# Performance work log

Hardware: AMD Instinct MI355X
Metric: run time of the kernel (lower is better)

## Reference

```python
import jax, jax.numpy as jnp
import numpy as np

B, CIN, NH, W, L, K = 16, 64, 64, 32, 4, 5
EPS = 1e-5
FORGET_BIAS = 1.0


def conv(x, w, b=None):
    # x: [B,C,H,W], w: [O,I,k,k] -> SAME padding, stride 1 (NCHW)
    y = jax.lax.conv_general_dilated(x, w, (1, 1), 'SAME',
                                     dimension_numbers=('NCHW', 'OIHW', 'NCHW'))
    if b is not None:
        y = y + b[None, :, None, None]
    return y


def ln(x, g, b):
    # torch LayerNorm([C,W,W]): normalize each sample over (C,H,W)
    m = jnp.mean(x, axis=(1, 2, 3), keepdims=True)
    v = jnp.mean((x - m) ** 2, axis=(1, 2, 3), keepdims=True)
    return (x - m) * jax.lax.rsqrt(v + EPS) * g[None] + b[None]


def attn_channel(q, kv):
    # q: [B,C,W,H], kv: [B,L,C,W,H]
    b, c, w, h = q.shape
    qf = q.reshape(b, c, w * h)                 # [B,C,HW]
    kf = kv.reshape(b, -1, w * h)               # [B,L*C,HW]
    a = jax.nn.softmax(jnp.einsum('bcp,blp->bcl', qf, kf), axis=2)  # [B,C,L*C]
    out = jnp.einsum('bcl,blp->bcp', a, kf)     # [B,C,HW]
    return out.reshape(b, c, w, h)


def attn_spatial(q, kv):
    # q: [B,C,W,H], kv: [B,L,C,W,H]
    b, c, w, h = q.shape
    qf = q.reshape(b, c, w * h).transpose(0, 2, 1)          # [B,HW,C]
    kf = kv.transpose(0, 1, 3, 4, 2).reshape(b, -1, c)      # [B,L*HW,C]
    a = jax.nn.softmax(jnp.einsum('bpc,bqc->bpq', qf, kf), axis=2)  # [B,HW,L*HW]
    out = jnp.einsum('bpq,bqc->bpc', a, kf)                 # [B,HW,C]
    return out.reshape(b, w, h, c).transpose(0, 3, 1, 2)


def setup_inputs() -> dict:
    key = jax.random.key(0)
    ks = iter(jax.random.split(key, 64))
    rn = lambda shape, s=1.0: jax.random.normal(next(ks), shape, jnp.float32) * s
    ones = lambda shape: jnp.ones(shape, jnp.float32)
    zeros = lambda shape: jnp.zeros(shape, jnp.float32)
    s = 0.02
    d = {}
    d['x_t'] = rn((B, CIN, W, W))
    d['h_t'] = rn((B, NH, W, W))
    d['c_t'] = rn((B, NH, W, W))
    d['c_historys'] = rn((B, L, NH, W, W))
    d['m_t'] = rn((B, NH, W, W))
    d['w_x'] = rn((7 * NH, CIN, K, K), s); d['ln_x_g'] = ones((7 * NH, W, W)); d['ln_x_b'] = zeros((7 * NH, W, W))
    d['w_h'] = rn((4 * NH, NH, K, K), s);  d['ln_h_g'] = ones((4 * NH, W, W)); d['ln_h_b'] = zeros((4 * NH, W, W))
    d['w_m'] = rn((3 * NH, NH, K, K), s);  d['ln_m_g'] = ones((3 * NH, W, W)); d['ln_m_b'] = zeros((3 * NH, W, W))
    d['w_o'] = rn((NH, 2 * NH, K, K), s);  d['ln_o_g'] = ones((NH, W, W));     d['ln_o_b'] = zeros((NH, W, W))
    d['w_last'] = rn((NH, 2 * NH, 1, 1), s)
    d['s_norm_g'] = ones((NH, W, W)); d['s_norm_b'] = zeros((NH, W, W))
    d['c_norm_g'] = ones((NH, W, W)); d['c_norm_b'] = zeros((NH, W, W))
    d['ca_w1'] = rn((NH, NH, K, K), s); d['ca_b1'] = zeros((NH,))
    d['ca_ln_g'] = ones((NH, W, W));    d['ca_ln_b'] = zeros((NH, W, W))
    d['ca_w2'] = rn((NH, NH, 1, 1), s); d['ca_b2'] = zeros((NH,))
    d['sa_w1'] = rn((NH, NH, K, K), s)
    d['sa_ln_g'] = ones((NH, W, W));    d['sa_ln_b'] = zeros((NH, W, W))
    d['sa_w2'] = rn((NH, NH, 1, 1), s)
    d['attn_w'] = rn((NH, NH, 1, 1), s)
    return d


def reference(x_t, h_t, c_t, c_historys, m_t,
              w_x, ln_x_g, ln_x_b, w_h, ln_h_g, ln_h_b, w_m, ln_m_g, ln_m_b,
              w_o, ln_o_g, ln_o_b, w_last,
              s_norm_g, s_norm_b, c_norm_g, c_norm_b,
              ca_w1, ca_b1, ca_ln_g, ca_ln_b, ca_w2, ca_b2,
              sa_w1, sa_ln_g, sa_ln_b, sa_w2, attn_w):
    x_concat = ln(conv(x_t, w_x), ln_x_g, ln_x_b)
    h_concat = ln(conv(h_t, w_h), ln_h_g, ln_h_b)
    m_concat = ln(conv(m_t, w_m), ln_m_g, ln_m_b)
    (i_x, f_x, g_x, i_xp, f_xp, g_xp, o_x) = jnp.split(x_concat, 7, axis=1)
    (i_h, f_h, g_h, o_h) = jnp.split(h_concat, 4, axis=1)
    (i_m, f_m, g_m) = jnp.split(m_concat, 3, axis=1)

    i_t = jax.nn.sigmoid(i_x + i_h)
    f_t = jax.nn.sigmoid(f_x + f_h + FORGET_BIAS)
    g_t = jnp.tanh(g_x + g_h)

    # attn_sum_fussion(c_t, query=f_t, keys=c_historys, values=c_historys)
    sp = ln(c_t + attn_spatial(f_t, c_historys), s_norm_g, s_norm_b)
    ch = ln(c_t + attn_channel(f_t, c_historys), c_norm_g, c_norm_b)
    s_a = conv(jax.nn.relu(ln(conv(sp, sa_w1), sa_ln_g, sa_ln_b)), sa_w2)
    c_a = conv(jax.nn.relu(ln(conv(ch, ca_w1, ca_b1), ca_ln_g, ca_ln_b)), ca_w2, ca_b2)
    attn = conv(s_a + c_a, attn_w)
    c_new = attn + i_t * g_t

    i_tp = jax.nn.sigmoid(i_xp + i_m)
    f_tp = jax.nn.sigmoid(f_xp + f_m + FORGET_BIAS)
    g_tp = jnp.tanh(g_xp + g_m)
    m_new = f_tp * m_t + i_tp * g_tp

    mem = jnp.concatenate((c_new, m_new), axis=1)
    o_t = jax.nn.sigmoid(o_x + o_h + ln(conv(mem, w_o), ln_o_g, ln_o_b))
    h_new = o_t * jnp.tanh(conv(mem, w_last))
    return h_new, c_new, m_new
```

## Files before the change

### kernel.cpp

```cpp
#include <hip/hip_runtime.h>
#include <hip/hip_bf16.h>

#define N1 (1u << 20)

typedef __attribute__((ext_vector_type(8))) short s8v;
typedef __attribute__((ext_vector_type(4))) float f4v;

static __device__ __forceinline__ float sigm(float x){ return 1.f/(1.f + __expf(-x)); }
static __device__ __forceinline__ float tanh_(float x){ return 1.f - 2.f/(__expf(2.f*x) + 1.f); }

static __device__ __forceinline__ ushort f2b(float f){
  union { float f; uint u; } x; x.f = f;
  uint r = x.u + 0x7FFFu + ((x.u >> 16) & 1u);
  return (ushort)(r >> 16);
}

static __device__ __forceinline__ void red_atomic2(float s, float q, float* d, int b, int t){
  #pragma unroll
  for (int m = 32; m; m >>= 1){ s += __shfl_xor(s, m); q += __shfl_xor(q, m); }
  if ((t & 63) == 0){ atomicAdd(&d[b*2], s); atomicAdd(&d[b*2+1], q); }
}

__global__ void k_zero(float* __restrict__ p){ p[threadIdx.x] = 0.f; }

__global__ __launch_bounds__(256) void k_wprep3(
    const float* __restrict__ sA, ushort* __restrict__ dA, int CoA, int CiA, int nA,
    const float* __restrict__ sB, ushort* __restrict__ dB, int CoB, int CiB, int nB,
    const float* __restrict__ sC, ushort* __restrict__ dC, int CoC, int CiC, int nC)
{
  int idx = blockIdx.x*256 + threadIdx.x;
  const float* s; ushort* d; int Co, Ci;
  if (idx < nA){ s=sA; d=dA; Co=CoA; Ci=CiA; }
  else if ((idx -= nA) < nB){ s=sB; d=dB; Co=CoB; Ci=CiB; }
  else if ((idx -= nB) < nC){ s=sC; d=dC; Co=CoC; Ci=CiC; }
  else return;
  int ci = idx % Ci; int r = idx / Ci; int co = r % Co; int tap = r / Co;
  d[idx] = f2b(s[((size_t)(co*Ci + ci))*25 + tap]);
}

struct PT { const float* s; ushort* d; const float* st; const float* g; const float* bb; };

__global__ __launch_bounds__(256) void k_prepT3(PT ja, PT jb, PT jc, int n0, int n1, float invN)
{
  const int lp = blockIdx.y;
  PT j; int pl;
  if (lp < n0){ j = ja; pl = lp; }
  else if (lp < n0 + n1){ j = jb; pl = lp - n0; }
  else { j = jc; pl = lp - n0 - n1; }
  const float* sp = j.s + ((size_t)pl << 16);
  float mean = 0.f, rstd = 0.f;
  if (j.st){
    float s0 = j.st[pl*2], s1 = j.st[pl*2+1];
    mean = s0*invN; rstd = rsqrtf(s1*invN - mean*mean + 1e-5f);
  }
  const int p0 = blockIdx.x << 6;
  __shared__ __align__(16) float T[64][68];
  const int t = threadIdx.x, c = t >> 2, g4 = t & 3;
  #pragma unroll
  for (int i = 0; i < 4; ++i){
    const int px = (g4 << 4) + (i << 2);
    float4 f = *(const float4*)(sp + ((size_t)c << 10) + p0 + px);
    if (j.st){
      const size_t li = ((size_t)c << 10) + p0 + px;
      float4 gv = *(const float4*)(j.g + li);
      float4 bv = *(const float4*)(j.bb + li);
      f.x = (f.x - mean)*rstd*gv.x + bv.x;
      f.y = (f.y - mean)*rstd*gv.y + bv.y;
      f.z = (f.z - mean)*rstd*gv.z + bv.z;
      f.w = (f.w - mean)*rstd*gv.w + bv.w;
    }
    *(float4*)&T[c][px] = f;
  }
  __syncthreads();
  const int p = t >> 2, c0 = (t & 3) << 4;
  uint w4[8];
  #pragma unroll
  for (int k = 0; k < 8; ++k){
    ushort lo = f2b(T[c0 + 2*k][p]);
    ushort hi = f2b(T[c0 + 2*k + 1][p]);
    w4[k] = (uint)lo | ((uint)hi << 16);
  }
  ushort* dst = j.d + ((((size_t)pl << 10) + p0 + p) << 6) + c0;
  *(uint4*)(dst)     = *(uint4*)&w4[0];
  *(uint4*)(dst + 8) = *(uint4*)&w4[4];
}

__global__ __launch_bounds__(256) void k_prepTm(const float* __restrict__ src, ushort* __restrict__ dT)
{
  const int lp = blockIdx.y;
  const int p0 = blockIdx.x << 6;
  const float* sp = src + ((size_t)lp << 16);
  __shared__ __align__(16) float T[64][68];
  const int t = threadIdx.x, c = t >> 2, g4 = t & 3;
  #pragma unroll
  for (int i = 0; i < 4; ++i){
    const int px = (g4 << 4) + (i << 2);
    *(float4*)&T[c][px] = *(const float4*)(sp + ((size_t)c << 10) + p0 + px);
  }
  __syncthreads();
  const int p = t >> 2, c0 = (t & 3) << 4;
  uint w4[8];
  #pragma unroll
  for (int k = 0; k < 8; ++k)
    w4[k] = (uint)f2b(T[c0 + 2*k][p]) | ((uint)f2b(T[c0 + 2*k + 1][p]) << 16);
  ushort* dst = dT + ((((size_t)(lp >> 1) << 10) + p0 + p) << 7) + ((lp & 1) << 6) + c0;
  *(uint4*)(dst)     = *(uint4*)&w4[0];
  *(uint4*)(dst + 8) = *(uint4*)&w4[4];
}

struct Seg {
  const ushort* inT; const ushort* w; const float* bias;
  float* out; float* ostat;
  int Cin, Cout;
};
struct Segs3 { Seg s[3]; int b1, b2; };

template<int MT>
__global__ __launch_bounds__(256, MT==4 ? 2 : 3) void k_convX(Segs3 Sg)
{
  constexpr int CO   = MT*16;
  constexpr int NW   = 5*CO*4;
  constexpr int ITW  = (NW + 255) / 256;
  constexpr int DXSH = (MT == 4 ? 8 : 7);

  const int b = blockIdx.y;
  const int cog = blockIdx.x >> 2, pxblk = blockIdx.x & 3;
  const int si = (cog >= Sg.b1) + (cog >= Sg.b2);
  const Seg sg = Sg.s[si];
  const int base = si == 0 ? 0 : (si == 1 ? Sg.b1 : Sg.b2);
  const int co0 = (cog - base) * CO;
  const int r0 = pxblk << 3;
  const int t = threadIdx.x, w = t >> 6, l = t & 63;
  const int lane16 = l & 15, quad = l >> 4;

  __shared__ __align__(16) ushort S_[4][12][36][8];
  __shared__ __align__(16) ushort W_[2][5*CO*32];

  f4v acc[MT][4];
  #pragma unroll
  for (int mi = 0; mi < MT; ++mi)
    #pragma unroll
    for (int n = 0; n < 4; ++n) acc[mi][n] = (f4v){0.f,0.f,0.f,0.f};

  size_t woff0[ITW];
  #pragma unroll
  for (int it = 0; it < ITW; ++it){
    const int u = t + it*256;
    const int l16u = u & 15, qu = (u >> 4) & 3;
    const int miu = (u >> 6) & (MT - 1), dxu = u >> DXSH;
    woff0[it] = ((size_t)(dxu*sg.Cout + co0 + miu*16 + l16u))*sg.Cin + (qu << 3);
  }
  const size_t wdy = (size_t)5 * sg.Cout * sg.Cin;

  const int ncc = sg.Cin >> 5;
  for (int cc = 0; cc < ncc; ++cc){
    __syncthreads();
    for (int idx = t; idx < 432; idx += 256){
      const int row = idx / 36, col = idx - row*36;
      const int ir = r0 - 2 + row, ic = col - 2;
      uint4 pk[4] = {make_uint4(0,0,0,0),make_uint4(0,0,0,0),make_uint4(0,0,0,0),make_uint4(0,0,0,0)};
      if ((unsigned)ir < 32u && (unsigned)ic < 32u){
        const ushort* bp = sg.inT + ((size_t)((b << 10) + (ir << 5) + ic)) * sg.Cin + (cc << 5);
        #pragma unroll
        for (int q = 0; q < 4; ++q) pk[q] = *(const uint4*)(bp + (q << 3));
      }
      #pragma unroll
      for (int q = 0; q < 4; ++q) *(uint4*)&S_[q][row][col][0] = pk[q];
    }
    {
      uint4 wreg[ITW];
      #pragma unroll
      for (int it = 0; it < ITW; ++it)
        if (ITW*256 == NW || t + it*256 < NW)
          wreg[it] = *(const uint4*)(sg.w + woff0[it] + (cc << 5));
      #pragma unroll
      for (int it = 0; it < ITW; ++it)
        if (ITW*256 == NW || t + it*256 < NW)
          *(uint4*)&W_[0][(size_t)(t + it*256) * 8] = wreg[it];
    }
    __syncthreads();
    #pragma unroll
    for (int dy = 0; dy < 5; ++dy){
      uint4 nreg[ITW];
      if (dy < 4){
        #pragma unroll
        for (int it = 0; it < ITW; ++it)
          if (ITW*256 == NW || t + it*256 < NW)
            nreg[it] = *(const uint4*)(sg.w + woff0[it] + (size_t)(dy+1)*wdy + (cc << 5));
      }
      #pragma unroll
      for (int dx = 0; dx < 5; ++dx){
        s8v a[MT];
        #pragma unroll
        for (int mi = 0; mi < MT; ++mi){
          const int au = ((((dx*MT + mi) << 2) + quad) << 4) + lane16;
          a[mi] = *(const s8v*)&W_[dy & 1][au << 3];
        }
        #pragma unroll
        for (int n = 0; n < 4; ++n){
          const int srow = (w << 1) + (n >> 1) + dy;
          const int col = ((n & 1) << 4) + lane16 + dx;
          s8v bb = *(const s8v*)&S_[quad][srow][col][0];
          #pragma unroll
          for (int mi = 0; mi < MT; ++mi)
            acc[mi][n] = __builtin_amdgcn_mfma_f32_16x16x32_bf16(a[mi], bb, acc[mi][n], 0, 0, 0);
        }
      }
      if (dy < 4){
        #pragma unroll
        for (int it = 0; it < ITW; ++it)
          if (ITW*256 == NW || t + it*256 < NW)
            *(uint4*)&W_[(dy+1) & 1][(size_t)(t + it*256) * 8] = nreg[it];
      }
      __syncthreads();
    }
  }
  float lsum = 0.f, lsq = 0.f;
  #pragma unroll
  for (int mi = 0; mi < MT; ++mi){
    const int co = co0 + mi*16 + (quad << 2);
    #pragma unroll
    for (int n = 0; n < 4; ++n){
      const int row = r0 + (w << 1) + (n >> 1);
      const int col = ((n & 1) << 4) + lane16;
      #pragma unroll
      for (int i = 0; i < 4; ++i){
        float v = acc[mi][n][i] + (sg.bias ? sg.bias[co+i] : 0.f);
        sg.out[(((size_t)(b*sg.Cout + co + i)) << 10) + (row << 5) + col] = v;
        lsum += v; lsq += v*v;
      }
    }
  }
  if (sg.ostat) red_atomic2(lsum, lsq, sg.ostat, b, t);
}

__global__ __launch_bounds__(256) void k_prep(const float* __restrict__ src,
                                              ushort* __restrict__ outC,
                                              ushort* __restrict__ outT)
{
  const int plane = blockIdx.y;
  const int p0 = blockIdx.x << 6;
  const float* sp = src + ((size_t)plane << 16);
  __shared__ __align__(16) float T[64][68];
  const int t = threadIdx.x, c = t >> 2, g = t & 3;
  #pragma unroll
  for (int i = 0; i < 4; ++i){
    float4 f = *(const float4*)(sp + ((size_t)c << 10) + p0 + (g << 4) + (i << 2));
    *(float4*)&T[c][(g << 4) + (i << 2)] = f;
    if (outC){
      uint2 pk2;
      pk2.x = (uint)f2b(f.x) | ((uint)f2b(f.y) << 16);
      pk2.y = (uint)f2b(f.z) | ((uint)f2b(f.w) << 16);
      *(uint2*)(outC + ((((size_t)plane << 6) + c) << 10) + p0 + (g << 4) + (i << 2)) = pk2;
    }
  }
  __syncthreads();
  const int p = t >> 2, c0 = (t & 3) << 4;
  uint w4[8];
  #pragma unroll
  for (int k = 0; k < 8; ++k){
    ushort lo = f2b(T[c0 + 2*k][p]);
    ushort hi = f2b(T[c0 + 2*k + 1][p]);
    w4[k] = (uint)lo | ((uint)hi << 16);
  }
  ushort* dst = outT + ((((size_t)plane << 10) + p0 + p) << 6) + c0;
  *(uint4*)(dst)     = *(uint4*)&w4[0];
  *(uint4*)(dst + 8) = *(uint4*)&w4[4];
}

__global__ __launch_bounds__(256) void k_gates(
    const float* __restrict__ bufx, const float* __restrict__ bufh, const float* __restrict__ bufm,
    const float* __restrict__ lnxg, const float* __restrict__ lnxb,
    const float* __restrict__ lnhg, const float* __restrict__ lnhb,
    const float* __restrict__ lnmg, const float* __restrict__ lnmb,
    const float* __restrict__ m_t, const float* __restrict__ stats,
    float* __restrict__ ft, float* __restrict__ ig, float* __restrict__ osum,
    float* __restrict__ memo, float* __restrict__ out_m)
{
  const int idx = blockIdx.x*256 + threadIdx.x;
  const int b = idx >> 16, rem = idx & 65535;
  const int c = rem >> 10, p = rem & 1023;

  float mx = stats[b*2]      * (1.f/458752.f);
  float vx = stats[b*2+1]    * (1.f/458752.f) - mx*mx;  float rx = rsqrtf(vx + 1e-5f);
  float mh = stats[32+b*2]   * (1.f/262144.f);
  float vh = stats[32+b*2+1] * (1.f/262144.f) - mh*mh;  float rh = rsqrtf(vh + 1e-5f);
  float mm = stats[64+b*2]   * (1.f/196608.f);
  float vm = stats[64+b*2+1] * (1.f/196608.f) - mm*mm;  float rm = rsqrtf(vm + 1e-5f);

  auto LX = [&](int k){
    size_t ch = (size_t)k*64 + c; size_t gi = ((size_t)b*448 + ch)*1024 + p; size_t li = ch*1024 + p;
    return (bufx[gi] - mx)*rx*lnxg[li] + lnxb[li]; };
  auto LH = [&](int k){
    size_t ch = (size_t)k*64 + c; size_t gi = ((size_t)b*256 + ch)*1024 + p; size_t li = ch*1024 + p;
    return (bufh[gi] - mh)*rh*lnhg[li] + lnhb[li]; };
  auto LM = [&](int k){
    size_t ch = (size_t)k*64 + c; size_t gi = ((size_t)b*192 + ch)*1024 + p; size_t li = ch*1024 + p;
    return (bufm[gi] - mm)*rm*lnmg[li] + lnmb[li]; };

  float i_t = sigm(LX(0) + LH(0));
  float f_t = sigm(LX(1) + LH(1) + 1.f);
  float g_t = tanh_(LX(2) + LH(2));
  float i_p = sigm(LX(3) + LM(0));
  float f_p = sigm(LX(4) + LM(1) + 1.f);
  float g_p = tanh_(LX(5) + LM(2));
  float ox = LX(6), oh = LH(3);

  ft[idx]   = f_t;
  ig[idx]   = i_t * g_t;
  osum[idx] = ox + oh;
  float mn = f_p * m_t[idx] + i_p * g_p;
  out_m[idx] = mn;
  memo[((size_t)(b*128 + 64 + c) << 10) + p] = mn;
}

__global__ __launch_bounds__(256) void k_spat_mfma(
    const ushort* __restrict__ qT, const ushort* __restrict__ kvC, const ushort* __restrict__ kvT,
    float* __restrict__ num0, float* __restrict__ num1, float* __restrict__ den)
{
  const int p0 = blockIdx.x << 6, b = blockIdx.y, half = blockIdx.z;
  const int t = threadIdx.x, w = t >> 6, l = t & 63;
  const int lane16 = l & 15, quad = l >> 4;
  __shared__ __align__(16) ushort Kt[64][72];
  __shared__ __align__(16) ushort Kc[64][72];
  __shared__ __align__(16) ushort Eb[64][72];
  __shared__ __align__(16) float  XO[64][65];

  s8v qa0, qa1;
  {
    const ushort* qr = qT + ((((size_t)b << 10) + p0 + (w << 4) + lane16) << 6) + (quad << 3);
    qa0 = *(const s8v*)(qr);
    qa1 = *(const s8v*)(qr + 32);
  }
  f4v o0 = {0.f,0.f,0.f,0.f}, o1 = o0, o2 = o0, o3 = o0, dacc = o0;
  const short oneb = (short)0x3F80;
  const s8v ones = { oneb, oneb, oneb, oneb, oneb, oneb, oneb, oneb };

  const int r = t >> 2, g4 = (t & 3) << 4;
  for (int ck = 0; ck < 32; ++ck){
    const int chunk = (half << 5) + ck;
    const int lidx = chunk >> 4, pk = (chunk & 15) << 6;
    __syncthreads();
    {
      const ushort* sc = kvC + ((((size_t)(b*4 + lidx) << 6) + r) << 10) + pk + g4;
      *(uint4*)&Kc[r][g4]     = *(const uint4*)(sc);
      *(uint4*)&Kc[r][g4 + 8] = *(const uint4*)(sc + 8);
      const ushort* st = kvT + ((((size_t)(b*4 + lidx) << 10) + pk + r) << 6) + g4;
      *(uint4*)&Kt[r][g4]     = *(const uint4*)(st);
      *(uint4*)&Kt[r][g4 + 8] = *(const uint4*)(st + 8);
    }
    __syncthreads();
    #pragma unroll
    for (int nt = 0; nt < 4; ++nt){
      const ushort* bt = &Kt[(nt << 4) + lane16][quad << 3];
      s8v b0 = *(const s8v*)(bt);
      s8v b1 = *(const s8v*)(bt + 32);
      f4v s = {0.f,0.f,0.f,0.f};
      s = __builtin_amdgcn_mfma_f32_16x16x32_bf16(qa0, b0, s, 0, 0, 0);
      s = __builtin_amdgcn_mfma_f32_16x16x32_bf16(qa1, b1, s, 0, 0, 0);
      #pragma unroll
      for (int i = 0; i < 4; ++i){
        float e = __expf(s[i] - 12.f);
        Eb[(w << 4) + (quad << 2) + i][(nt << 4) + lane16] = f2b(e);
      }
    }
    __syncthreads();
    #pragma unroll
    for (int ks = 0; ks < 2; ++ks){
      s8v ea = *(const s8v*)&Eb[(w << 4) + lane16][(ks << 5) + (quad << 3)];
      dacc = __builtin_amdgcn_mfma_f32_16x16x32_bf16(ea, ones, dacc, 0, 0, 0);
      s8v bc0 = *(const s8v*)&Kc[ 0 + lane16][(ks << 5) + (quad << 3)];
      s8v bc1 = *(const s8v*)&Kc[16 + lane16][(ks << 5) + (quad << 3)];
      s8v bc2 = *(const s8v*)&Kc[32 + lane16][(ks << 5) + (quad << 3)];
      s8v bc3 = *(const s8v*)&Kc[48 + lane16][(ks << 5) + (quad << 3)];
      o0 = __builtin_amdgcn_mfma_f32_16x16x32_bf16(ea, bc0, o0, 0, 0, 0);
      o1 = __builtin_amdgcn_mfma_f32_16x16x32_bf16(ea, bc1, o1, 0, 0, 0);
      o2 = __builtin_amdgcn_mfma_f32_16x16x32_bf16(ea, bc2, o2, 0, 0, 0);
      o3 = __builtin_amdgcn_mfma_f32_16x16x32_bf16(ea, bc3, o3, 0, 0, 0);
    }
  }
  {
    const int pxl = (w << 4) + (quad << 2);
    if (lane16 == 0){
      float* dp = den + (((size_t)(half*16 + b)) << 10) + p0 + pxl;
      dp[0] = dacc[0]; dp[1] = dacc[1]; dp[2] = dacc[2]; dp[3] = dacc[3];
    }
    XO[ 0 + lane16][pxl+0] = o0[0]; XO[ 0 + lane16][pxl+1] = o0[1];
    XO[ 0 + lane16][pxl+2] = o0[2]; XO[ 0 + lane16][pxl+3] = o0[3];
    XO[16 + lane16][pxl+0] = o1[0]; XO[16 + lane16][pxl+1] = o1[1];
    XO[16 + lane16][pxl+2] = o1[2]; XO[16 + lane16][pxl+3] = o1[3];
    XO[32 + lane16][pxl+0] = o2[0]; XO[32 + lane16][pxl+1] = o2[1];
    XO[32 + lane16][pxl+2] = o2[2]; XO[32 + lane16][pxl+3] = o2[3];
    XO[48 + lane16][pxl+0] = o3[0]; XO[48 + lane16][pxl+1] = o3[1];
    XO[48 + lane16][pxl+2] = o3[2]; XO[48 + lane16][pxl+3] = o3[3];
  }
  __syncthreads();
  {
    const int ch = t >> 2;
    float* nout = half ? num1 : num0;
    #pragma unroll
    for (int i = 0; i < 4; ++i){
      size_t gi = ((size_t)b << 16) + ((size_t)ch << 10) + p0 + g4 + (i << 2);
      float4 ov;
      ov.x = XO[ch][g4 + (i << 2) + 0];
      ov.y = XO[ch][g4 + (i << 2) + 1];
      ov.z = XO[ch][g4 + (i << 2) + 2];
      ov.w = XO[ch][g4 + (i << 2) + 3];
      *(float4*)(nout + gi) = ov;
    }
  }
}

__global__ __launch_bounds__(256) void k_spcomb(
    const float* num0, const float* num1, const float* __restrict__ den,
    const float* __restrict__ c_t, float* sp_raw, float* __restrict__ stats)
{
  const int p0 = blockIdx.x << 6, b = blockIdx.y, t = threadIdx.x;
  const int ch = t >> 2, g4 = (t & 3) << 4;
  float lsum = 0.f, lsq = 0.f;
  #pragma unroll
  for (int i = 0; i < 4; ++i){
    const int px = p0 + g4 + (i << 2);
    size_t gi = ((size_t)b << 16) + ((size_t)ch << 10) + px;
    float4 n0 = *(const float4*)(num0 + gi);
    float4 n1 = *(const float4*)(num1 + gi);
    float4 cv = *(const float4*)(c_t + gi);
    const float* d0 = den + (((size_t)b) << 10) + px;
    const float* d1 = den + (((size_t)(16 + b)) << 10) + px;
    float4 ov;
    ov.x = cv.x + (n0.x + n1.x) / (d0[0] + d1[0]);
    ov.y = cv.y + (n0.y + n1.y) / (d0[1] + d1[1]);
    ov.z = cv.z + (n0.z + n1.z) / (d0[2] + d1[2]);
    ov.w = cv.w + (n0.w + n1.w) / (d0[3] + d1[3]);
    *(float4*)(sp_raw + gi) = ov;
    lsum += ov.x + ov.y + ov.z + ov.w;
    lsq  += ov.x*ov.x + ov.y*ov.y + ov.z*ov.z + ov.w*ov.w;
  }
  red_atomic2(lsum, lsq, stats, b, t);
}

__global__ __launch_bounds__(256) void k_chlog_m(
    const ushort* __restrict__ ftC, const ushort* __restrict__ kvC, float* __restrict__ lg)
{
  const int bx = blockIdx.x, b = blockIdx.y;
  const int np = bx >> 1, mp = bx & 1;
  const int t = threadIdx.x, w = t >> 6, l = t & 63;
  const int lane16 = l & 15, quad = l >> 4;
  __shared__ __align__(16) ushort As[8][32][8];
  __shared__ __align__(16) ushort Bs[8][64][8];
  f4v acc[2];
  acc[0] = (f4v){0.f,0.f,0.f,0.f}; acc[1] = (f4v){0.f,0.f,0.f,0.f};

  for (int kc = 0; kc < 16; ++kc){
    __syncthreads();
    {
      const int c = t >> 3, q = t & 7;
      *(uint4*)&As[q][c][0] = *(const uint4*)(ftC + (((size_t)(b*64 + mp*32 + c)) << 10) + (kc<<6) + (q<<3));
    }
    #pragma unroll
    for (int it = 0; it < 2; ++it){
      const int idx = t + it*256;
      const int r2 = idx >> 3, q = idx & 7;
      *(uint4*)&Bs[q][r2][0] = *(const uint4*)(kvC + ((((size_t)(b*4 + np) << 6) + r2) << 10) + (kc<<6) + (q<<3));
    }
    __syncthreads();
    #pragma unroll
    for (int ks = 0; ks < 2; ++ks){
      s8v a0 = *(const s8v*)&As[(ks<<2)+quad][lane16][0];
      s8v a1 = *(const s8v*)&As[(ks<<2)+quad][16 + lane16][0];
      s8v bb = *(const s8v*)&Bs[(ks<<2)+quad][(w<<4) + lane16][0];
      acc[0] = __builtin_amdgcn_mfma_f32_16x16x32_bf16(a0, bb, acc[0], 0, 0, 0);
      acc[1] = __builtin_amdgcn_mfma_f32_16x16x32_bf16(a1, bb, acc[1], 0, 0, 0);
    }
  }
  #pragma unroll
  for (int mi = 0; mi < 2; ++mi)
    #pragma unroll
    for (int i = 0; i < 4; ++i){
      const int c = mp*32 + mi*16 + (quad<<2) + i;
      const int n = (np<<6) + (w<<4) + lane16;
      lg[(((size_t)(b*64 + c)) << 8) + n] = acc[mi][i];
    }
}

__global__ __launch_bounds__(256) void k_chsm(const float* __restrict__ a, ushort* __restrict__ ab)
{
  const int row  = blockIdx.x*4 + (threadIdx.x >> 6);
  const int lane = threadIdx.x & 63;
  const float* rp = a + ((size_t)row << 8);
  float v0 = rp[lane], v1 = rp[lane+64], v2 = rp[lane+128], v3 = rp[lane+192];
  float mx = fmaxf(fmaxf(v0, v1), fmaxf(v2, v3));
  #pragma unroll
  for (int m = 32; m; m >>= 1) mx = fmaxf(mx, __shfl_xor(mx, m));
  v0 = __expf(v0 - mx); v1 = __expf(v1 - mx); v2 = __expf(v2 - mx); v3 = __expf(v3 - mx);
  float s = v0 + v1 + v2 + v3;
  #pragma unroll
  for (int m = 32; m; m >>= 1) s += __shfl_xor(s, m);
  float inv = 1.f / s;
  ushort* op = ab + ((size_t)row << 8);
  op[lane] = f2b(v0*inv); op[lane+64] = f2b(v1*inv);
  op[lane+128] = f2b(v2*inv); op[lane+192] = f2b(v3*inv);
}

__global__ __launch_bounds__(256) void k_chout_m(
    const ushort* __restrict__ chlb, const ushort* __restrict__ kvT,
    const float* __restrict__ c_t, float* __restrict__ ch_raw, float* __restrict__ stats)
{
  const int p0 = blockIdx.x << 6, b = blockIdx.y;
  const int t = threadIdx.x, w = t >> 6, l = t & 63;
  const int lane16 = l & 15, quad = l >> 4;
  __shared__ __align__(16) ushort As[32][64][8];
  __shared__ __align__(16) ushort Bs[32][32][8];
  #pragma unroll
  for (int it = 0; it < 8; ++it){
    const int idx = t + it*256;
    const int c = idx >> 5, q = idx & 31;
    *(uint4*)&As[q][c][0] = *(const uint4*)(chlb + (((size_t)(b*64 + c)) << 8) + (q<<3));
  }
  __syncthreads();
  s8v a[8];
  #pragma unroll
  for (int ks = 0; ks < 8; ++ks)
    a[ks] = *(const s8v*)&As[(ks<<2)+quad][(w<<4) + lane16][0];
  float lsum = 0.f, lsq = 0.f;
  for (int pc = 0; pc < 2; ++pc){
    __syncthreads();
    #pragma unroll
    for (int it = 0; it < 4; ++it){
      const int idx = t + it*256;
      const int px = idx >> 5, q = idx & 31;
      const int plane = (b<<2) + (q>>3);
      *(uint4*)&Bs[q][px][0] = *(const uint4*)(kvT + ((((size_t)plane << 10) + p0 + (pc<<5) + px) << 6) + ((q&7)<<3));
    }
    __syncthreads();
    #pragma unroll
    for (int nt = 0; nt < 2; ++nt){
      f4v o = {0.f,0.f,0.f,0.f};
      #pragma unroll
      for (int ks = 0; ks < 8; ++ks){
        s8v bb = *(const s8v*)&Bs[(ks<<2)+quad][(nt<<4) + lane16][0];
        o = __builtin_amdgcn_mfma_f32_16x16x32_bf16(a[ks], bb, o, 0, 0, 0);
      }
      #pragma unroll
      for (int i = 0; i < 4; ++i){
        const int c = (w<<4) + (quad<<2) + i;
        const int px = p0 + (pc<<5) + (nt<<4) + lane16;
        size_t gi = ((size_t)b << 16) + ((size_t)c << 10) + px;
        float v = c_t[gi] + o[i];
        ch_raw[gi] = v;
        lsum += v; lsq += v*v;
      }
    }
  }
  red_atomic2(lsum, lsq, stats, b, t);
}

__global__ __launch_bounds__(256) void k_attnfinal(
    const float* __restrict__ samid, const float* __restrict__ camid,
    const float* __restrict__ stats_sa, const float* __restrict__ stats_ca,
    const float* __restrict__ salng, const float* __restrict__ salnb,
    const float* __restrict__ calng, const float* __restrict__ calnb,
    const float* __restrict__ wsa2, const float* __restrict__ wca2,
    const float* __restrict__ cab2, const float* __restrict__ wat,
    const float* __restrict__ ig, float* __restrict__ out_c, float* __restrict__ memo)
{
  const int p0 = blockIdx.x << 6, b = blockIdx.y, t = threadIdx.x;
  const int tc = t & 15, tp = t >> 4;
  __shared__ __align__(16) float R[64][68];
  __shared__ __align__(16) float Wl[64][68];
  __shared__ __align__(16) float Ms[64][68];
  const float invN = 1.f/65536.f;
  float acc[4][4] = {};
  #pragma unroll
  for (int pass = 0; pass < 2; ++pass){
    const float* mid = pass ? camid : samid;
    const float* st  = pass ? stats_ca : stats_sa;
    const float* g   = pass ? calng : salng;
    const float* bb  = pass ? calnb : salnb;
    const float* w   = pass ? wca2  : wsa2;
    float mean = st[b*2]*invN;
    float var  = st[b*2+1]*invN - mean*mean;
    float rstd = rsqrtf(var + 1e-5f);
    __syncthreads();
    {
      const int j = t & 63, c0 = t >> 6;
      for (int ci = c0; ci < 64; ci += 4){
        size_t gi = ((size_t)b << 16) + ((size_t)ci << 10) + p0 + j;
        size_t li = ((size_t)ci << 10) + p0 + j;
        float v = (mid[gi] - mean)*rstd*g[li] + bb[li];
        R[ci][j] = fmaxf(v, 0.f);
      }
      const int ci2 = t & 63, c20 = t >> 6;
      for (int c2 = c20; c2 < 64; c2 += 4) Wl[ci2][c2] = w[((size_t)c2 << 6) + ci2];
    }
    __syncthreads();
    for (int ci = 0; ci < 64; ++ci){
      float wv[4], rv[4];
      *(float4*)wv = *(const float4*)&Wl[ci][4*tc];
      *(float4*)rv = *(const float4*)&R[ci][4*tp];
      #pragma unroll
      for (int i = 0; i < 4; ++i)
        #pragma unroll
        for (int j = 0; j < 4; ++j)
          acc[i][j] = fmaf(wv[i], rv[j], acc[i][j]);
    }
  }
  {
    float b2[4];
    #pragma unroll
    for (int i = 0; i < 4; ++i) b2[i] = cab2[4*tc + i];
    #pragma unroll
    for (int i = 0; i < 4; ++i)
      #pragma unroll
      for (int j = 0; j < 4; ++j)
        Ms[4*tc+i][4*tp+j] = acc[i][j] + b2[i];
  }
  __syncthreads();
  {
    const int ci2 = t & 63, c20 = t >> 6;
    for (int c2 = c20; c2 < 64; c2 += 4) Wl[ci2][c2] = wat[((size_t)c2 << 6) + ci2];
  }
  __syncthreads();
  float acc2[4][4] = {};
  for (int c2 = 0; c2 < 64; ++c2){
    float wv[4], mv[4];
    *(float4*)wv = *(const float4*)&Wl[c2][4*tc];
    *(float4*)mv = *(const float4*)&Ms[c2][4*tp];
    #pragma unroll
    for (int i = 0; i < 4; ++i)
      #pragma unroll
      for (int j = 0; j < 4; ++j)
        acc2[i][j] = fmaf(wv[i], mv[j], acc2[i][j]);
  }
  #pragma unroll
  for (int i = 0; i < 4; ++i)
    #pragma unroll
    for (int j = 0; j < 4; ++j){
      size_t gi = ((size_t)b << 16) + ((size_t)(4*tc + i) << 10) + p0 + 4*tp + j;
      float v = acc2[i][j] + ig[gi];
      out_c[gi] = v;
      memo[((size_t)(b*128 + 4*tc + i) << 10) + p0 + 4*tp + j] = v;
    }
}

__global__ __launch_bounds__(256) void k_final(
    const float* __restrict__ memo, const float* __restrict__ wlast,
    const float* __restrict__ bufo, const float* __restrict__ osum,
    const float* __restrict__ stats_o, const float* __restrict__ lnog, const float* __restrict__ lnob,
    float* __restrict__ out_h)
{
  const int p0 = blockIdx.x << 6, b = blockIdx.y, t = threadIdx.x;
  const int tc = t & 15, tp = t >> 4;
  __shared__ __align__(16) float Msh[64][68];
  __shared__ __align__(16) float Wt[64][68];
  float acc[4][4] = {};
  #pragma unroll
  for (int half = 0; half < 2; ++half){
    __syncthreads();
    {
      const int j = t & 63, c0 = t >> 6;
      for (int ci = c0; ci < 64; ci += 4)
        Msh[ci][j] = memo[((size_t)(b*128 + half*64 + ci) << 10) + p0 + j];
      const int ci2 = t & 63, co0 = t >> 6;
      for (int co = co0; co < 64; co += 4) Wt[ci2][co] = wlast[((size_t)co << 7) + half*64 + ci2];
    }
    __syncthreads();
    for (int ci = 0; ci < 64; ++ci){
      float wv[4], mv[4];
      *(float4*)wv = *(const float4*)&Wt[ci][4*tc];
      *(float4*)mv = *(const float4*)&Msh[ci][4*tp];
      #pragma unroll
      for (int i = 0; i < 4; ++i)
        #pragma unroll
        for (int j = 0; j < 4; ++j)
          acc[i][j] = fmaf(wv[i], mv[j], acc[i][j]);
    }
  }
  float mean = stats_o[b*2]*(1.f/65536.f);
  float var  = stats_o[b*2+1]*(1.f/65536.f) - mean*mean;
  float rstd = rsqrtf(var + 1e-5f);
  #pragma unroll
  for (int i = 0; i < 4; ++i)
    #pragma unroll
    for (int j = 0; j < 4; ++j){
      const int co = 4*tc + i, p = p0 + 4*tp + j;
      size_t gi = ((size_t)b << 16) + ((size_t)co << 10) + p;
      size_t li = ((size_t)co << 10) + p;
      float lno = (bufo[gi] - mean)*rstd*lnog[li] + lnob[li];
      float o = sigm(osum[gi] + lno);
      out_h[gi] = o * tanh_(acc[i][j]);
    }
}

extern "C" void kernel_launch(void* const* d_in, const int* in_sizes, int n_in,
                              void* d_out, int out_size, void* d_ws, size_t ws_size,
                              hipStream_t stream)
{
  const float* x_t   = (const float*)d_in[0];
  const float* h_t   = (const float*)d_in[1];
  const float* c_t   = (const float*)d_in[2];
  const float* chist = (const float*)d_in[3];
  const float* m_t   = (const float*)d_in[4];
  const float* w_x   = (const float*)d_in[5];
  const float* lnxg  = (const float*)d_in[6];
  const float* lnxb  = (const float*)d_in[7];
  const float* w_h   = (const float*)d_in[8];
  const float* lnhg  = (const float*)d_in[9];
  const float* lnhb  = (const float*)d_in[10];
  const float* w_m   = (const float*)d_in[11];
  const float* lnmg  = (const float*)d_in[12];
  const float* lnmb  = (const float*)d_in[13];
  const float* w_o   = (const float*)d_in[14];
  const float* lnog  = (const float*)d_in[15];
  const float* lnob  = (const float*)d_in[16];
  const float* w_last= (const float*)d_in[17];
  const float* sng   = (const float*)d_in[18];
  const float* snb   = (const float*)d_in[19];
  const float* cng   = (const float*)d_in[20];
  const float* cnb   = (const float*)d_in[21];
  const float* ca_w1 = (const float*)d_in[22];
  const float* ca_b1 = (const float*)d_in[23];
  const float* calng = (const float*)d_in[24];
  const float* calnb = (const float*)d_in[25];
  const float* ca_w2 = (const float*)d_in[26];
  const float* ca_b2 = (const float*)d_in[27];
  const float* sa_w1 = (const float*)d_in[28];
  const float* salng = (const float*)d_in[29];
  const float* salnb = (const float*)d_in[30];
  const float* sa_w2 = (const float*)d_in[31];
  const float* attn_w= (const float*)d_in[32];

  float* out = (float*)d_out;
  float* ws  = (float*)d_ws;

  float* stats = ws;
  float* bufx  = ws + 1024;
  float* bufh  = bufx + 7*(size_t)N1;
  float* bufm  = bufh + 4*(size_t)N1;
  float* ft    = bufm + 3*(size_t)N1;
  float* ig    = ft   + (size_t)N1;
  float* osum  = ig   + (size_t)N1;
  float* memo  = osum + (size_t)N1;
  float* sp    = bufx;
  float* ch    = bufx + (size_t)N1;
  float* samid = bufx + 2*(size_t)N1;
  float* camid = bufx + 3*(size_t)N1;
  float* bufo  = bufx + 4*(size_t)N1;
  float* chl   = bufx + 5*(size_t)N1;
  ushort* kvC  = (ushort*)bufh;
  ushort* kvT  = kvC + 4*(size_t)N1;
  ushort* qT   = (ushort*)bufm;
  ushort* ftC  = qT + (size_t)N1;

  ushort* xT   = (ushort*)memo;
  ushort* hT   = xT + (size_t)N1;
  ushort* mT   = hT + (size_t)N1;
  ushort* spT  = ftC + (size_t)N1;
  ushort* chT  = spT + (size_t)N1;
  float*  num1 = bufm + 2*(size_t)N1;
  float*  denP = chl;
  ushort* memoT = (ushort*)bufx;

  ushort* wbx = (ushort*)ft;
  ushort* wbh = wbx + 716800;
  ushort* wbm = wbh + 409600;
  ushort* wbo  = (ushort*)(chl + 262144);
  ushort* wbsa = wbo + 204800;
  ushort* wbca = wbsa + 102400;
  ushort* chlb = wbca + 102400;

  float* out_h = out;
  float* out_c = out + (size_t)N1;
  float* out_m = out + 2*(size_t)N1;

  k_zero<<<dim3(1), dim3(256), 0, stream>>>(stats);

  k_wprep3<<<dim3(5600), dim3(256), 0, stream>>>(
      w_x, wbx, 448, 64, 716800,
      w_h, wbh, 256, 64, 409600,
      w_m, wbm, 192, 64, 307200);

  {
    PT jx{ x_t, xT, nullptr, nullptr, nullptr };
    PT jh{ h_t, hT, nullptr, nullptr, nullptr };
    PT jm{ m_t, mT, nullptr, nullptr, nullptr };
    k_prepT3<<<dim3(16,48), dim3(256), 0, stream>>>(jx, jh, jm, 16, 16, 0.f);
  }

  {
    Segs3 XHM;
    XHM.s[0] = Seg{ xT, wbx, nullptr, bufx, stats+0,  64, 448 };
    XHM.s[1] = Seg{ hT, wbh, nullptr, bufh, stats+32, 64, 256 };
    XHM.s[2] = Seg{ mT, wbm, nullptr, bufm, stats+64, 64, 192 };
    XHM.b1 = 7; XHM.b2 = 11;
    k_convX<4><<<dim3(56,16), dim3(256), 0, stream>>>(XHM);
  }

  k_gates<<<dim3(4096), dim3(256), 0, stream>>>(bufx, bufh, bufm, lnxg, lnxb, lnhg, lnhb,
                                                lnmg, lnmb, m_t, stats,
                                                ft, ig, osum, memo, out_m);

  k_wprep3<<<dim3(1600), dim3(256), 0, stream>>>(
      w_o,   wbo,  64, 128, 204800,
      sa_w1, wbsa, 64,  64, 102400,
      ca_w1, wbca, 64,  64, 102400);

  k_prep<<<dim3(16,64), dim3(256), 0, stream>>>(chist, kvC, kvT);
  k_prep<<<dim3(16,16), dim3(256), 0, stream>>>(ft, ftC, qT);

  k_spat_mfma<<<dim3(16,16,2), dim3(256), 0, stream>>>(qT, kvC, kvT, sp, num1, denP);
  k_spcomb<<<dim3(16,16), dim3(256), 0, stream>>>(sp, num1, denP, c_t, sp, stats+96);

  k_chlog_m<<<dim3(8,16), dim3(256), 0, stream>>>(ftC, kvC, chl);
  k_chsm  <<<dim3(256),  dim3(256), 0, stream>>>(chl, chlb);
  k_chout_m<<<dim3(16,16), dim3(256), 0, stream>>>(chlb, kvT, c_t, ch, stats+128);

  {
    PT js{ sp, spT, stats+96,  sng, snb };
    PT jc{ ch, chT, stats+128, cng, cnb };
    k_prepT3<<<dim3(16,32), dim3(256), 0, stream>>>(js, jc, js, 16, 16, 1.f/65536.f);
  }

  {
    Segs3 SC;
    SC.s[0] = Seg{ spT, wbsa, nullptr, samid, stats+160, 64, 64 };
    SC.s[1] = Seg{ chT, wbca, ca_b1,   camid, stats+192, 64, 64 };
    SC.s[2] = SC.s[1];
    SC.b1 = 2; SC.b2 = 1000;
    k_convX<2><<<dim3(16,16), dim3(256), 0, stream>>>(SC);
  }

  k_attnfinal<<<dim3(16,16), dim3(256), 0, stream>>>(samid, camid, stats+160, stats+192,
                                                     salng, salnb, calng, calnb,
                                                     sa_w2, ca_w2, ca_b2, attn_w,
                                                     ig, out_c, memo);

  k_prepTm<<<dim3(16,32), dim3(256), 0, stream>>>(memo, memoT);

  {
    Segs3 O;
    O.s[0] = Seg{ memoT, wbo, nullptr, bufo, stats+224, 128, 64 };
    O.s[1] = O.s[0]; O.s[2] = O.s[0];
    O.b1 = 1000; O.b2 = 1000;
    k_convX<2><<<dim3(8,16), dim3(256), 0, stream>>>(O);
  }

  k_final<<<dim3(16,16), dim3(256), 0, stream>>>(memo, w_last, bufo, osum, stats+224,
                                                 lnog, lnob, out_h);
}
```

Measured before the change: 496.8 us.

## Increase grid parallelism for small convs and spatial attention, merge prep launches

Templates the conv kernel on rows-per-block so the two small 64-output convs run with half-height tiles and twice as many blocks. Splits the spatial attention key range four ways instead of two and sums the four partial numerators and denominators in the combine kernel. Folds the stats zeroing into the weight-prep kernel and merges the two transpose/prep launches into one. This targets under-filled GPUs and launch overhead, but costs more halo reloading per block and more partial-sum traffic and buffer space.

Result: no change. 501.7 us (+1.0%).

```diff
diff --git a/kernel.cpp b/kernel.cpp
--- a/kernel.cpp
+++ b/kernel.cpp
@@ -21,13 +21,13 @@
   if ((t & 63) == 0){ atomicAdd(&d[b*2], s); atomicAdd(&d[b*2+1], q); }
 }
 
-__global__ void k_zero(float* __restrict__ p){ p[threadIdx.x] = 0.f; }
-
 __global__ __launch_bounds__(256) void k_wprep3(
     const float* __restrict__ sA, ushort* __restrict__ dA, int CoA, int CiA, int nA,
     const float* __restrict__ sB, ushort* __restrict__ dB, int CoB, int CiB, int nB,
-    const float* __restrict__ sC, ushort* __restrict__ dC, int CoC, int CiC, int nC)
-{
+    const float* __restrict__ sC, ushort* __restrict__ dC, int CoC, int CiC, int nC,
+    float* __restrict__ zs)
+{
+  if (zs && blockIdx.x == 0) zs[threadIdx.x] = 0.f;
   int idx = blockIdx.x*256 + threadIdx.x;
   const float* s; ushort* d; int Co, Ci;
   if (idx < nA){ s=sA; d=dA; Co=CoA; Ci=CiA; }
@@ -115,32 +115,37 @@
 };
 struct Segs3 { Seg s[3]; int b1, b2; };
 
-template<int MT>
+template<int MT, int RPB>
 __global__ __launch_bounds__(256, MT==4 ? 2 : 3) void k_convX(Segs3 Sg)
 {
   constexpr int CO   = MT*16;
   constexpr int NW   = 5*CO*4;
   constexpr int ITW  = (NW + 255) / 256;
   constexpr int DXSH = (MT == 4 ? 8 : 7);
+  constexpr int PXB  = 32/RPB;
+  constexpr int ROWS = RPB + 4;
+  constexpr int RPW  = RPB/4;
+  constexpr int NTIL = RPB/2;
+  constexpr int SUN2 = ROWS*36;
 
   const int b = blockIdx.y;
-  const int cog = blockIdx.x >> 2, pxblk = blockIdx.x & 3;
+  const int cog = blockIdx.x / PXB, pxblk = blockIdx.x % PXB;
   const int si = (cog >= Sg.b1) + (cog >= Sg.b2);
   const Seg sg = Sg.s[si];
   const int base = si == 0 ? 0 : (si == 1 ? Sg.b1 : Sg.b2);
   const int co0 = (cog - base) * CO;
-  const int r0 = pxblk << 3;
+  const int r0 = pxblk * RPB;
   const int t = threadIdx.x, w = t >> 6, l = t & 63;
   const int lane16 = l & 15, quad = l >> 4;
 
-  __shared__ __align__(16) ushort S_[4][12][36][8];
+  __shared__ __align__(16) ushort S_[4][ROWS][36][8];
   __shared__ __align__(16) ushort W_[2][5*CO*32];
 
-  f4v acc[MT][4];
+  f4v acc[MT][NTIL];
   #pragma unroll
   for (int mi = 0; mi < MT; ++mi)
     #pragma unroll
-    for (int n = 0; n < 4; ++n) acc[mi][n] = (f4v){0.f,0.f,0.f,0.f};
+    for (int n = 0; n < NTIL; ++n) acc[mi][n] = (f4v){0.f,0.f,0.f,0.f};
 
   size_t woff0[ITW];
   #pragma unroll
@@ -155,7 +160,7 @@
   const int ncc = sg.Cin >> 5;
   for (int cc = 0; cc < ncc; ++cc){
     __syncthreads();
-    for (int idx = t; idx < 432; idx += 256){
+    for (int idx = t; idx < SUN2; idx += 256){
       const int row = idx / 36, col = idx - row*36;
       const int ir = r0 - 2 + row, ic = col - 2;
       uint4 pk[4] = {make_uint4(0,0,0,0),make_uint4(0,0,0,0),make_uint4(0,0,0,0),make_uint4(0,0,0,0)};
@@ -197,8 +202,8 @@
           a[mi] = *(const s8v*)&W_[dy & 1][au << 3];
         }
         #pragma unroll
-        for (int n = 0; n < 4; ++n){
-          const int srow = (w << 1) + (n >> 1) + dy;
+        for (int n = 0; n < NTIL; ++n){
+          const int srow = w*RPW + (n >> 1) + dy;
           const int col = ((n & 1) << 4) + lane16 + dx;
           s8v bb = *(const s8v*)&S_[quad][srow][col][0];
           #pragma unroll
@@ -220,8 +225,8 @@
   for (int mi = 0; mi < MT; ++mi){
     const int co = co0 + mi*16 + (quad << 2);
     #pragma unroll
-    for (int n = 0; n < 4; ++n){
-      const int row = r0 + (w << 1) + (n >> 1);
+    for (int n = 0; n < NTIL; ++n){
+      const int row = r0 + w*RPW + (n >> 1);
       const int col = ((n & 1) << 4) + lane16;
       #pragma unroll
       for (int i = 0; i < 4; ++i){
@@ -234,25 +239,26 @@
   if (sg.ostat) red_atomic2(lsum, lsq, sg.ostat, b, t);
 }
 
-__global__ __launch_bounds__(256) void k_prep(const float* __restrict__ src,
-                                              ushort* __restrict__ outC,
-                                              ushort* __restrict__ outT)
+__global__ __launch_bounds__(256) void k_prep2(
+    const float* __restrict__ sA, ushort* __restrict__ cA, ushort* __restrict__ tA, int nA,
+    const float* __restrict__ sB, ushort* __restrict__ cB, ushort* __restrict__ tB)
 {
   const int plane = blockIdx.y;
+  const float* src; ushort* outC; ushort* outT; int pl;
+  if (plane < nA){ src = sA; outC = cA; outT = tA; pl = plane; }
+  else { src = sB; outC = cB; outT = tB; pl = plane - nA; }
   const int p0 = blockIdx.x << 6;
-  const float* sp = src + ((size_t)plane << 16);
+  const float* sp = src + ((size_t)pl << 16);
   __shared__ __align__(16) float T[64][68];
   const int t = threadIdx.x, c = t >> 2, g = t & 3;
   #pragma unroll
   for (int i = 0; i < 4; ++i){
     float4 f = *(const float4*)(sp + ((size_t)c << 10) + p0 + (g << 4) + (i << 2));
     *(float4*)&T[c][(g << 4) + (i << 2)] = f;
-    if (outC){
-      uint2 pk2;
-      pk2.x = (uint)f2b(f.x) | ((uint)f2b(f.y) << 16);
-      pk2.y = (uint)f2b(f.z) | ((uint)f2b(f.w) << 16);
-      *(uint2*)(outC + ((((size_t)plane << 6) + c) << 10) + p0 + (g << 4) + (i << 2)) = pk2;
-    }
+    uint2 pk2;
+    pk2.x = (uint)f2b(f.x) | ((uint)f2b(f.y) << 16);
+    pk2.y = (uint)f2b(f.z) | ((uint)f2b(f.w) << 16);
+    *(uint2*)(outC + ((((size_t)pl << 6) + c) << 10) + p0 + (g << 4) + (i << 2)) = pk2;
   }
   __syncthreads();
   const int p = t >> 2, c0 = (t & 3) << 4;
@@ -263,7 +269,7 @@
     ushort hi = f2b(T[c0 + 2*k + 1][p]);
     w4[k] = (uint)lo | ((uint)hi << 16);
   }
-  ushort* dst = outT + ((((size_t)plane << 10) + p0 + p) << 6) + c0;
+  ushort* dst = outT + ((((size_t)pl << 10) + p0 + p) << 6) + c0;
   *(uint4*)(dst)     = *(uint4*)&w4[0];
   *(uint4*)(dst + 8) = *(uint4*)&w4[4];
 }
@@ -316,7 +322,7 @@
 
 __global__ __launch_bounds__(256) void k_spat_mfma(
     const ushort* __restrict__ qT, const ushort* __restrict__ kvC, const ushort* __restrict__ kvT,
-    float* __restrict__ num0, float* __restrict__ num1, float* __restrict__ den)
+    float* __restrict__ num, float* __restrict__ den)
 {
   const int p0 = blockIdx.x << 6, b = blockIdx.y, half = blockIdx.z;
   const int t = threadIdx.x, w = t >> 6, l = t & 63;
@@ -337,8 +343,8 @@
   const s8v ones = { oneb, oneb, oneb, oneb, oneb, oneb, oneb, oneb };
 
   const int r = t >> 2, g4 = (t & 3) << 4;
-  for (int ck = 0; ck < 32; ++ck){
-    const int chunk = (half << 5) + ck;
+  for (int ck = 0; ck < 16; ++ck){
+    const int chunk = (half << 4) + ck;
     const int lidx = chunk >> 4, pk = (chunk & 15) << 6;
     __syncthreads();
     {
@@ -397,7 +403,7 @@
   __syncthreads();
   {
     const int ch = t >> 2;
-    float* nout = half ? num1 : num0;
+    float* nout = num + (size_t)half * N1;
     #pragma unroll
     for (int i = 0; i < 4; ++i){
       size_t gi = ((size_t)b << 16) + ((size_t)ch << 10) + p0 + g4 + (i << 2);
@@ -412,7 +418,7 @@
 }
 
 __global__ __launch_bounds__(256) void k_spcomb(
-    const float* num0, const float* num1, const float* __restrict__ den,
+    const float* num, const float* __restrict__ den,
     const float* __restrict__ c_t, float* sp_raw, float* __restrict__ stats)
 {
   const int p0 = blockIdx.x << 6, b = blockIdx.y, t = threadIdx.x;
@@ -422,16 +428,21 @@
   for (int i = 0; i < 4; ++i){
     const int px = p0 + g4 + (i << 2);
     size_t gi = ((size_t)b << 16) + ((size_t)ch << 10) + px;
-    float4 n0 = *(const float4*)(num0 + gi);
-    float4 n1 = *(const float4*)(num1 + gi);
+    float4 ns = {0.f,0.f,0.f,0.f};
+    float d0 = 0.f, d1 = 0.f, d2 = 0.f, d3 = 0.f;
+    #pragma unroll
+    for (int k = 0; k < 4; ++k){
+      float4 nk = *(const float4*)(num + (size_t)k*N1 + gi);
+      ns.x += nk.x; ns.y += nk.y; ns.z += nk.z; ns.w += nk.w;
+      const float* dp = den + (((size_t)(k*16 + b)) << 10) + px;
+      d0 += dp[0]; d1 += dp[1]; d2 += dp[2]; d3 += dp[3];
+    }
     float4 cv = *(const float4*)(c_t + gi);
-    const float* d0 = den + (((size_t)b) << 10) + px;
-    const float* d1 = den + (((size_t)(16 + b)) << 10) + px;
     float4 ov;
-    ov.x = cv.x + (n0.x + n1.x) / (d0[0] + d1[0]);
-    ov.y = cv.y + (n0.y + n1.y) / (d0[1] + d1[1]);
-    ov.z = cv.z + (n0.z + n1.z) / (d0[2] + d1[2]);
-    ov.w = cv.w + (n0.w + n1.w) / (d0[3] + d1[3]);
+    ov.x = cv.x + ns.x / d0;
+    ov.y = cv.y + ns.y / d1;
+    ov.z = cv.z + ns.z / d2;
+    ov.w = cv.w + ns.w / d3;
     *(float4*)(sp_raw + gi) = ov;
     lsum += ov.x + ov.y + ov.z + ov.w;
     lsq  += ov.x*ov.x + ov.y*ov.y + ov.z*ov.z + ov.w*ov.w;
@@ -757,7 +768,7 @@
   ushort* mT   = hT + (size_t)N1;
   ushort* spT  = ftC + (size_t)N1;
   ushort* chT  = spT + (size_t)N1;
-  float*  num1 = bufm + 2*(size_t)N1;
+  float*  numB = bufx;
   float*  denP = chl;
   ushort* memoT = (ushort*)bufx;
 
@@ -773,12 +784,10 @@
   float* out_c = out + (size_t)N1;
   float* out_m = out + 2*(size_t)N1;
 
-  k_zero<<<dim3(1), dim3(256), 0, stream>>>(stats);
-
   k_wprep3<<<dim3(5600), dim3(256), 0, stream>>>(
       w_x, wbx, 448, 64, 716800,
       w_h, wbh, 256, 64, 409600,
-      w_m, wbm, 192, 64, 307200);
+      w_m, wbm, 192, 64, 307200, stats);
 
   {
     PT jx{ x_t, xT, nullptr, nullptr, nullptr };
@@ -793,7 +802,7 @@
     XHM.s[1] = Seg{ hT, wbh, nullptr, bufh, stats+32, 64, 256 };
     XHM.s[2] = Seg{ mT, wbm, nullptr, bufm, stats+64, 64, 192 };
     XHM.b1 = 7; XHM.b2 = 11;
-    k_convX<4><<<dim3(56,16), dim3(256), 0, stream>>>(XHM);
+    k_convX<4,8><<<dim3(56,16), dim3(256), 0, stream>>>(XHM);
   }
 
   k_gates<<<dim3(4096), dim3(256), 0, stream>>>(bufx, bufh, bufm, lnxg, lnxb, lnhg, lnhb,
@@ -803,13 +812,12 @@
   k_wprep3<<<dim3(1600), dim3(256), 0, stream>>>(
       w_o,   wbo,  64, 128, 204800,
       sa_w1, wbsa, 64,  64, 102400,
-      ca_w1, wbca, 64,  64, 102400);
-
-  k_prep<<<dim3(16,64), dim3(256), 0, stream>>>(chist, kvC, kvT);
-  k_prep<<<dim3(16,16), dim3(256), 0, stream>>>(ft, ftC, qT);
-
-  k_spat_mfma<<<dim3(16,16,2), dim3(256), 0, stream>>>(qT, kvC, kvT, sp, num1, denP);
-  k_spcomb<<<dim3(16,16), dim3(256), 0, stream>>>(sp, num1, denP, c_t, sp, stats+96);
+      ca_w1, wbca, 64,  64, 102400, nullptr);
+
+  k_prep2<<<dim3(16,80), dim3(256), 0, stream>>>(chist, kvC, kvT, 64, ft, ftC, qT);
+
+  k_spat_mfma<<<dim3(16,16,4), dim3(256), 0, stream>>>(qT, kvC, kvT, numB, denP);
+  k_spcomb<<<dim3(16,16), dim3(256), 0, stream>>>(numB, denP, c_t, sp, stats+96);
 
   k_chlog_m<<<dim3(8,16), dim3(256), 0, stream>>>(ftC, kvC, chl);
   k_chsm  <<<dim3(256),  dim3(256), 0, stream>>>(chl, chlb);
@@ -827,7 +835,7 @@
     SC.s[1] = Seg{ chT, wbca, ca_b1,   camid, stats+192, 64, 64 };
     SC.s[2] = SC.s[1];
     SC.b1 = 2; SC.b2 = 1000;
-    k_convX<2><<<dim3(16,16), dim3(256), 0, stream>>>(SC);
+    k_convX<2,4><<<dim3(32,16), dim3(256), 0, stream>>>(SC);
   }
 
   k_attnfinal<<<dim3(16,16), dim3(256), 0, stream>>>(samid, camid, stats+160, stats+192,
@@ -842,7 +850,7 @@
     O.s[0] = Seg{ memoT, wbo, nullptr, bufo, stats+224, 128, 64 };
     O.s[1] = O.s[0]; O.s[2] = O.s[0];
     O.b1 = 1000; O.b2 = 1000;
-    k_convX<2><<<dim3(8,16), dim3(256), 0, stream>>>(O);
+    k_convX<2,4><<<dim3(16,16), dim3(256), 0, stream>>>(O);
   }
 
   k_final<<<dim3(16,16), dim3(256), 0, stream>>>(memo, w_last, bufo, osum, stats+224,
```
